# Optimization experiments

Measured on AMD Instinct MI355X. Metric: run time of the kernel, lower is better.

Reference implementation:

```python
import jax, jax.numpy as jnp
import numpy as np

NUM_CLASSES = 80
SCORE_THRESH = 0.5
NMS_THRESH = 0.5
TOP_K = 200  # max candidates kept per (image, class) before greedy NMS


def setup_inputs() -> dict:
    key = jax.random.key(0)
    k1, k2, k3 = jax.random.split(key, 3)
    B, A, HW, C = 8, 3, 5776, NUM_CLASSES  # 608-input YOLOv4 P3 level: 76*76
    # well-formed boxes in [0,1]: x1y1 + positive wh
    xy = jax.random.uniform(k1, (B, A, HW, 2)) * 0.8
    wh = jax.random.uniform(k2, (B, A, HW, 2)) * 0.2 + 0.01
    boxes = jnp.concatenate([xy, xy + wh], axis=-1)
    scores = jax.random.uniform(k3, (B, A, HW, C))
    return {"boxes": boxes, "scores": scores}


def _pairwise_iou(b):
    # b: [K, 4] (x1, y1, x2, y2) -> IoU matrix [K, K] (union mode)
    x1, y1, x2, y2 = b[:, 0], b[:, 1], b[:, 2], b[:, 3]
    area = (x2 - x1) * (y2 - y1)
    xx1 = jnp.maximum(x1[:, None], x1[None, :])
    yy1 = jnp.maximum(y1[:, None], y1[None, :])
    xx2 = jnp.minimum(x2[:, None], x2[None, :])
    yy2 = jnp.minimum(y2[:, None], y2[None, :])
    inter = jnp.maximum(0.0, xx2 - xx1) * jnp.maximum(0.0, yy2 - yy1)
    return inter / (area[:, None] + area[None, :] - inter)


def _nms_one(boxes, scores):
    # boxes: [N, 4], scores: [N] -> top-K candidates with greedy-NMS keep mask
    s = jnp.where(scores > SCORE_THRESH, scores, -jnp.inf)  # score threshold filter
    top_s, idx = jax.lax.top_k(s, TOP_K)                    # descending, like argsort()[::-1]
    b = boxes[idx]                                          # [K, 4]
    valid = jnp.isfinite(top_s)
    iou = _pairwise_iou(b)                                  # [K, K]

    def body(keep, i):
        # if box i survives, suppress all lower-scored boxes with IoU > thresh
        sup = keep[i] & (iou[i] > NMS_THRESH) & (jnp.arange(TOP_K) > i)
        return keep & ~sup, None

    keep, _ = jax.lax.scan(body, valid, jnp.arange(TOP_K))
    return b, top_s, keep


def reference(boxes, scores):
    B, A, HW, _ = boxes.shape
    C = scores.shape[-1]
    b = boxes.reshape(B, A * HW, 4)
    s = scores.reshape(B, A * HW, C)
    per_img = jax.vmap(lambda bb, ss: jax.vmap(_nms_one, in_axes=(None, 1))(bb, ss))
    boxes_k, scores_k, keep = per_img(b, s)  # [B,C,K,4], [B,C,K], [B,C,K]
    cls = jnp.broadcast_to(jnp.arange(C, dtype=boxes.dtype)[None, :, None], keep.shape)
    out_box = jnp.where(keep[..., None], boxes_k, 0.0)
    out_score = jnp.where(keep, scores_k, 0.0)
    out_cls = jnp.where(keep, cls, 0.0)
    # padded detections [B, C, K, 6] = (x1, y1, x2, y2, score, class_id)
    return jnp.concatenate([out_box, out_score[..., None], out_cls[..., None]], axis=-1)
```

## Files before the change

### kernel.cpp

```cpp
#include <hip/hip_runtime.h>
#include <stdint.h>

#define B_IMG  8
#define NANCH  17328
#define NCLS   80
#define TOPK   200
#define NTHR   256
#define NTHRB  512
#define CHUNK  64
#define NCHK   ((NANCH + CHUNK - 1) / CHUNK)
#define NCHKP  272
#define SLOT   12
#define NPOS   (NCHK * SLOT)
#define NBC    (B_IMG * NCLS)
#define THRESH_HI 0.98f

__device__ __forceinline__ void hist_add(float s, unsigned int* hist) {
  if (s > 0.5f) {
    unsigned int bin = (__float_as_uint(s) - 0x3F000000u) >> 15;
    if (bin > 255u) bin = 255u;
    atomicAdd(&hist[bin], 1u);
  }
}

__global__ __launch_bounds__(NTHR) void scatter_k(
    const float* __restrict__ scores,
    unsigned char* __restrict__ cnt2,
    unsigned long long* __restrict__ cand) {
  const int nb = blockIdx.x;
  const int b  = blockIdx.y;
  const int tid = threadIdx.x;
  const int wv = tid >> 6, lane = tid & 63;
  const int n0 = nb * CHUNK;

  __shared__ float tile[CHUNK][81];

  const int nrow = (NANCH - n0 < CHUNK) ? (NANCH - n0) : CHUNK;
  const int nf4 = nrow * (NCLS / 4);
  const float4* src4 = (const float4*)(scores + (size_t)(b * NANCH + n0) * NCLS);
  for (int f = tid; f < nf4; f += NTHR) {
    float4 v = src4[f];
    int n = f / 20, c4 = (f - n * 20) * 4;
    tile[n][c4] = v.x; tile[n][c4 + 1] = v.y;
    tile[n][c4 + 2] = v.z; tile[n][c4 + 3] = v.w;
  }
  __syncthreads();

  const bool rv = (lane < nrow);
  const unsigned long long lt = (1ull << lane) - 1ull;
  const int cbase = wv * 20;
#pragma unroll 4
  for (int cc = 0; cc < 20; ++cc) {
    const int c = cbase + cc;
    const int bc = b * NCLS + c;
    float s = rv ? tile[lane][c] : 0.f;
    const bool cd = (s > THRESH_HI);
    unsigned long long bal = __ballot(cd);
    if (cd) {
      unsigned int r = (unsigned int)__popcll(bal & lt);
      if (r < SLOT)
        cand[((size_t)bc * NCHK + nb) * SLOT + r] =
            ((unsigned long long)__float_as_uint(s) << 32) |
            (unsigned long long)(0xFFFFFFFFu - (unsigned int)(n0 + lane));
    }
    if (lane == 0)
      cnt2[(size_t)bc * NCHKP + nb] = (unsigned char)__popcll(bal);
  }
}

__global__ __launch_bounds__(NTHR) void select_k(
    const float* __restrict__ scores, const float* __restrict__ boxes,
    const unsigned char* __restrict__ cnt2, const unsigned long long* __restrict__ cand,
    float4* __restrict__ stagedBox, unsigned long long* __restrict__ stagedKey) {
  const int bc = blockIdx.x;
  const int b = bc / NCLS;
  const int c = bc - b * NCLS;
  const int tid = threadIdx.x;
  const int lane = tid & 63;
  const unsigned long long lt = (1ull << lane) - 1ull;

  __shared__ unsigned long long selk[512];
  __shared__ unsigned int hist[256];
  __shared__ unsigned int sh_cutbits;
  __shared__ int sh_sel, sh_bad;

  if (tid == 0) { sh_sel = 0; sh_bad = 0; }
  __syncthreads();

  const unsigned long long* cb0 = cand + (size_t)bc * NCHK * SLOT;
  const unsigned char* ct0 = cnt2 + (size_t)bc * NCHKP;
  for (int p = tid; p < NPOS; p += NTHR) {
    const int ch = p / SLOT;
    const int sl = p - ch * SLOT;
    unsigned int ci = (unsigned int)ct0[ch];
    if (sl == 0 && ci > SLOT) sh_bad = 1;
    unsigned long long k = 0ull;
    bool pred = (sl < (int)ci);
    if (pred) k = cb0[p];
    unsigned long long bal = __ballot(pred);
    if (bal) {
      int base0 = 0;
      if (lane == 0) base0 = atomicAdd(&sh_sel, (int)__popcll(bal));
      base0 = __shfl(base0, 0, 64);
      if (pred) {
        int pos = base0 + (int)__popcll(bal & lt);
        if (pos < 512) selk[pos] = k;
      }
    }
  }
  __syncthreads();

  int Msel = sh_sel;
  const bool fb = (sh_bad != 0) || (Msel < TOPK) || (Msel > 512);

  if (fb) {
    if (tid < 256) hist[tid] = 0u;
    if (tid == 0) sh_sel = 0;
    __syncthreads();
    const float* src = scores + (size_t)b * NANCH * NCLS + c;
    for (int i = tid; i < NANCH; i += NTHR) hist_add(src[(size_t)i * NCLS], hist);
    __syncthreads();
    if (tid == 0) {
      unsigned int acc = 0;
      int cut = 0;
      for (int bin = 255; bin >= 0; --bin) {
        acc += hist[bin];
        if (acc >= TOPK) { cut = bin; break; }
      }
      sh_cutbits = 0x3F000000u + ((unsigned int)cut << 15);
    }
    __syncthreads();
    const unsigned int cutbits = sh_cutbits;
    for (int i = tid; i < NANCH; i += NTHR) {
      float s = src[(size_t)i * NCLS];
      if (s > 0.5f && __float_as_uint(s) >= cutbits) {
        int slot = atomicAdd(&sh_sel, 1);
        if (slot < 512)
          selk[slot] = ((unsigned long long)__float_as_uint(s) << 32) |
                       (unsigned long long)(0xFFFFFFFFu - (unsigned int)i);
      }
    }
    __syncthreads();
    Msel = sh_sel; if (Msel > 512) Msel = 512;
  }

  const int S = (Msel <= 256) ? 256 : 512;
  for (int j = Msel + tid; j < S; j += NTHR) selk[j] = 0ull;

  for (int size = 2; size <= S; size <<= 1) {
    for (int st = size >> 1; st > 0; st >>= 1) {
      __syncthreads();
      for (int t = tid; t < (S >> 1); t += NTHR) {
        int lo = 2 * t - (t & (st - 1));
        int hi = lo + st;
        bool desc = ((lo & size) == 0);
        unsigned long long a = selk[lo], bb = selk[hi];
        if ((a < bb) == desc) { selk[lo] = bb; selk[hi] = a; }
      }
    }
  }
  __syncthreads();

  {
    unsigned long long key = selk[tid];
    int valid = (tid < TOPK) && (key != 0ull);
    unsigned int idx = 0xFFFFFFFFu - (unsigned int)(key & 0xFFFFFFFFull);
    float4 bx = make_float4(0.f, 0.f, 0.f, 0.f);
    if (valid) bx = ((const float4*)boxes)[(size_t)b * NANCH + idx];
    stagedBox[(size_t)bc * 256 + tid] = bx;
    stagedKey[(size_t)bc * 256 + tid] = valid ? key : 0ull;
  }
}

__global__ __launch_bounds__(NTHRB) void nms_k(
    const float4* __restrict__ stagedBox, const unsigned long long* __restrict__ stagedKey,
    float* __restrict__ out) {
  const int bc = blockIdx.x;
  const int c = bc - (bc / NCLS) * NCLS;
  const int tid = threadIdx.x;
  const int wv = tid >> 6, lane = tid & 63;

  __shared__ float sx1[256], sy1[256], sx2[256], sy2[256], sar[256], ssc[256];
  __shared__ int skeep[256];
  __shared__ __align__(16) unsigned long long sup[TOPK][4];
  __shared__ __align__(16) float eout[TOPK * 6];

  if (tid < 256) {
    unsigned long long key = stagedKey[(size_t)bc * 256 + tid];
    float4 bx = stagedBox[(size_t)bc * 256 + tid];
    int valid = (tid < TOPK) && (key != 0ull);
    sx1[tid] = bx.x; sy1[tid] = bx.y; sx2[tid] = bx.z; sy2[tid] = bx.w;
    sar[tid] = __fmul_rn(bx.z - bx.x, bx.w - bx.y);
    ssc[tid] = valid ? __uint_as_float((unsigned int)(key >> 32)) : 0.f;
    skeep[tid] = valid;
  }
  __syncthreads();

  {
    float jx1[4], jy1[4], jx2[4], jy2[4], ja[4];
#pragma unroll
    for (int r = 0; r < 4; ++r) {
      int j = (r << 6) | lane;
      jx1[r] = sx1[j]; jy1[r] = sy1[j]; jx2[r] = sx2[j]; jy2[r] = sy2[j];
      ja[r] = sar[j];
    }
    float nx1 = sx1[wv], ny1 = sy1[wv], nx2 = sx2[wv], ny2 = sy2[wv], na = sar[wv];
    for (int k = 0; k < 25; ++k) {
      const int i = (k << 3) + wv;
      const float xi1 = nx1, yi1 = ny1, xi2 = nx2, yi2 = ny2, ai = na;
      const int inx = i + 8;
      if (inx < TOPK) {
        nx1 = sx1[inx]; ny1 = sy1[inx]; nx2 = sx2[inx]; ny2 = sy2[inx];
        na = sar[inx];
      }
      const int d = i >> 6;
      const int il = i & 63;
      unsigned long long dmask = (il == 63) ? 0ull : ((~0ull) << (il + 1));
      if (d == 3) dmask &= 0xFFull;
      unsigned long long w[4];
#pragma unroll
      for (int r = 0; r < 4; ++r) {
        unsigned long long word = 0ull;
        if ((r << 6) + 63 > i) {
          const unsigned long long wmask =
              (r > d) ? ((r == 3) ? 0xFFull : ~0ull) : dmask;
          float xx1 = fmaxf(xi1, jx1[r]);
          float yy1 = fmaxf(yi1, jy1[r]);
          float xx2 = fminf(xi2, jx2[r]);
          float yy2 = fminf(yi2, jy2[r]);
          float iw = fmaxf(0.f, __fsub_rn(xx2, xx1));
          float ih = fmaxf(0.f, __fsub_rn(yy2, yy1));
          float inter = __fmul_rn(iw, ih);
          float denom = __fsub_rn(__fadd_rn(ai, ja[r]), inter);
          float i2 = __fadd_rn(inter, inter);
          word = __ballot(i2 > denom);
          unsigned long long gb =
              __ballot((i2 > denom) &&
                       (i2 <= __fmul_rn(denom, 1.0000005f))) & wmask;
          if (gb)
            word = __ballot(__fdiv_rn(inter, denom) > 0.5f);
          word &= wmask;
        }
        w[r] = word;
      }
      if (lane == 0) {
        ulonglong2* dst = (ulonglong2*)&sup[i][0];
        ulonglong2 t0; t0.x = w[0]; t0.y = w[1];
        ulonglong2 t1; t1.x = w[2]; t1.y = w[3];
        dst[0] = t0; dst[1] = t1;
      }
    }
  }
  __syncthreads();

  if (tid < 64) {
    unsigned long long k0 = __ballot(skeep[tid] != 0);
    unsigned long long k1 = __ballot(skeep[64 + tid] != 0);
    unsigned long long k2 = __ballot(skeep[128 + tid] != 0);
    unsigned long long k3 = __ballot(skeep[192 + tid] != 0);
#define NMS_SCAN_WORD(KW, BASE, CNT)                                     \
    _Pragma("unroll 8")                                                  \
    for (int li = 0; li < (CNT); ++li) {                                 \
      const ulonglong2* s2p =                                            \
          reinterpret_cast<const ulonglong2*>(&sup[(BASE) + li][0]);     \
      ulonglong2 sa = s2p[0];                                            \
      ulonglong2 sb = s2p[1];                                            \
      unsigned long long m = 0ull - ((KW >> li) & 1ull);                 \
      k0 &= ~(sa.x & m); k1 &= ~(sa.y & m);                              \
      k2 &= ~(sb.x & m); k3 &= ~(sb.y & m);                              \
    }
    NMS_SCAN_WORD(k0, 0, 64)
    NMS_SCAN_WORD(k1, 64, 64)
    NMS_SCAN_WORD(k2, 128, 64)
    NMS_SCAN_WORD(k3, 192, 8)
#undef NMS_SCAN_WORD
    skeep[tid]        = (int)((k0 >> tid) & 1ull);
    skeep[64 + tid]   = (int)((k1 >> tid) & 1ull);
    skeep[128 + tid]  = (int)((k2 >> tid) & 1ull);
    skeep[192 + tid]  = (int)((k3 >> tid) & 1ull);
  }
  __syncthreads();

  if (tid < TOPK) {
    int kp = skeep[tid];
    eout[tid * 6 + 0] = kp ? sx1[tid] : 0.f;
    eout[tid * 6 + 1] = kp ? sy1[tid] : 0.f;
    eout[tid * 6 + 2] = kp ? sx2[tid] : 0.f;
    eout[tid * 6 + 3] = kp ? sy2[tid] : 0.f;
    eout[tid * 6 + 4] = kp ? ssc[tid] : 0.f;
    eout[tid * 6 + 5] = kp ? (float)c : 0.f;
  }
  __syncthreads();

  float4* out4 = (float4*)(out + (size_t)bc * (TOPK * 6));
  const float4* e4 = (const float4*)eout;
  for (int f = tid; f < (TOPK * 6) / 4; f += NTHRB) out4[f] = e4[f];
}

__global__ __launch_bounds__(NTHR) void select_nms_k(
    const float* __restrict__ boxes, const float* __restrict__ scores,
    float* __restrict__ out) {
  const int blk = blockIdx.x;
  const int b = blk / NCLS;
  const int c = blk - b * NCLS;
  const int tid = threadIdx.x;

  __shared__ unsigned int hist[256];
  __shared__ unsigned long long keys[1024];
  __shared__ float sx1[TOPK], sy1[TOPK], sx2[TOPK], sy2[TOPK], sar[TOPK], ssc[TOPK];
  __shared__ int skeep[TOPK];
  __shared__ unsigned int sh_cutbits;
  __shared__ int sh_m;

  const float* src = scores + (size_t)b * NANCH * NCLS + c;

  for (int j = tid; j < 256; j += NTHR) hist[j] = 0;
  if (tid == 0) sh_m = 0;
  __syncthreads();

  for (int i = tid; i < NANCH; i += NTHR) hist_add(src[(size_t)i * NCLS], hist);
  __syncthreads();

  if (tid == 0) {
    unsigned int acc = 0;
    int cut = 0;
    for (int bin = 255; bin >= 0; --bin) {
      acc += hist[bin];
      if (acc >= TOPK) { cut = bin; break; }
    }
    sh_cutbits = 0x3F000000u + ((unsigned int)cut << 15);
  }
  __syncthreads();
  const unsigned int cutbits = sh_cutbits;

  for (int i = tid; i < NANCH; i += NTHR) {
    float s = src[(size_t)i * NCLS];
    if (s > 0.5f && __float_as_uint(s) >= cutbits) {
      int slot = atomicAdd(&sh_m, 1);
      if (slot < 1024)
        keys[slot] = ((unsigned long long)__float_as_uint(s) << 32) |
                     (unsigned long long)(0xFFFFFFFFu - (unsigned int)i);
    }
  }
  __syncthreads();
  int M = sh_m; if (M > 1024) M = 1024;
  for (int j = M + tid; j < 1024; j += NTHR) keys[j] = 0ull;

  for (int size = 2; size <= 1024; size <<= 1) {
    for (int st = size >> 1; st > 0; st >>= 1) {
      __syncthreads();
      for (int t = tid; t < 512; t += NTHR) {
        int lo = 2 * t - (t & (st - 1));
        int hi = lo + st;
        bool desc = ((lo & size) == 0);
        unsigned long long a = keys[lo], bb = keys[hi];
        if ((a < bb) == desc) { keys[lo] = bb; keys[hi] = a; }
      }
    }
  }
  __syncthreads();

  if (tid < TOPK) {
    unsigned long long key = keys[tid];
    int valid = (key != 0ull);
    float sc = __uint_as_float((unsigned int)(key >> 32));
    unsigned int idx = 0xFFFFFFFFu - (unsigned int)(key & 0xFFFFFFFFull);
    float4 bx = make_float4(0.f, 0.f, 0.f, 0.f);
    if (valid) bx = ((const float4*)boxes)[(size_t)b * NANCH + idx];
    sx1[tid] = bx.x; sy1[tid] = bx.y; sx2[tid] = bx.z; sy2[tid] = bx.w;
    sar[tid] = __fmul_rn(bx.z - bx.x, bx.w - bx.y);
    ssc[tid] = valid ? sc : 0.f;
    skeep[tid] = valid;
  }
  __syncthreads();

  if (tid < 64) {
    const int lane = tid;
    float x1v[4], y1v[4], x2v[4], y2v[4], av[4];
    int km = 0;
#pragma unroll
    for (int r = 0; r < 4; ++r) {
      int j = lane + (r << 6);
      if (j < TOPK) {
        x1v[r] = sx1[j]; y1v[r] = sy1[j]; x2v[r] = sx2[j]; y2v[r] = sy2[j];
        av[r] = sar[j];
        if (skeep[j]) km |= (1 << r);
      } else {
        x1v[r] = 0.f; y1v[r] = 0.f; x2v[r] = 0.f; y2v[r] = 0.f; av[r] = 0.f;
      }
    }
#pragma unroll
    for (int ri = 0; ri < 4; ++ri) {
      const int imax = (ri == 3) ? (TOPK - 192) : 64;
      for (int li = 0; li < imax; ++li) {
        const int i = (ri << 6) + li;
        int kmi = __shfl(km, li, 64);
        if (!((kmi >> ri) & 1)) continue;
        float xi1 = __shfl(x1v[ri], li, 64);
        float yi1 = __shfl(y1v[ri], li, 64);
        float xi2 = __shfl(x2v[ri], li, 64);
        float yi2 = __shfl(y2v[ri], li, 64);
        float ai  = __shfl(av[ri],  li, 64);
#pragma unroll
        for (int r = 0; r < 4; ++r) {
          int j = lane + (r << 6);
          if (j > i && j < TOPK && ((km >> r) & 1)) {
            float xx1 = fmaxf(xi1, x1v[r]);
            float yy1 = fmaxf(yi1, y1v[r]);
            float xx2 = fminf(xi2, x2v[r]);
            float yy2 = fminf(yi2, y2v[r]);
            float iw = fmaxf(0.f, __fsub_rn(xx2, xx1));
            float ih = fmaxf(0.f, __fsub_rn(yy2, yy1));
            float inter = __fmul_rn(iw, ih);
            float denom = __fsub_rn(__fadd_rn(ai, av[r]), inter);
            float iou = __fdiv_rn(inter, denom);
            if (iou > 0.5f) km &= ~(1 << r);
          }
        }
      }
    }
#pragma unroll
    for (int r = 0; r < 4; ++r) {
      int j = lane + (r << 6);
      if (j < TOPK) skeep[j] = (km >> r) & 1;
    }
  }
  __syncthreads();

  const size_t base = ((size_t)b * NCLS + c) * (TOPK * 6);
  for (int f = tid; f < TOPK * 6; f += NTHR) {
    int k = f / 6, comp = f - k * 6;
    float v = 0.f;
    if (skeep[k]) {
      switch (comp) {
        case 0: v = sx1[k]; break;
        case 1: v = sy1[k]; break;
        case 2: v = sx2[k]; break;
        case 3: v = sy2[k]; break;
        case 4: v = ssc[k]; break;
        default: v = (float)c; break;
      }
    }
    out[base + f] = v;
  }
}

extern "C" void kernel_launch(void* const* d_in, const int* in_sizes, int n_in,
                              void* d_out, int out_size, void* d_ws, size_t ws_size,
                              hipStream_t stream) {
  (void)in_sizes; (void)n_in; (void)out_size;
  const float* boxes  = (const float*)d_in[0];
  const float* scores = (const float*)d_in[1];
  float* out = (float*)d_out;

  const size_t need_c2 = (size_t)NBC * NCHKP;
  const size_t need_cd = (size_t)NBC * NCHK * SLOT * sizeof(uint64_t);
  const size_t need_sb = (size_t)NBC * 256 * sizeof(float4);
  const size_t need_sk = (size_t)NBC * 256 * sizeof(uint64_t);
  const size_t need = need_c2 + need_cd + need_sb + need_sk;

  if (ws_size >= need) {
    char* w = (char*)d_ws;
    unsigned char* cnt2           = (unsigned char*)w;       w += need_c2;
    unsigned long long* cand      = (unsigned long long*)w;  w += need_cd;
    float4* stagedBox             = (float4*)w;              w += need_sb;
    unsigned long long* stagedKey = (unsigned long long*)w;

    scatter_k<<<dim3(NCHK, B_IMG), NTHR, 0, stream>>>(scores, cnt2, cand);
    select_k<<<NBC, NTHR, 0, stream>>>(scores, boxes, cnt2, cand,
                                       stagedBox, stagedKey);
    nms_k<<<NBC, NTHRB, 0, stream>>>(stagedBox, stagedKey, out);
  } else {
    select_nms_k<<<NBC, NTHR, 0, stream>>>(boxes, scores, out);
  }
}
```

Before: 79.71 us.

## Split NMS into separate suppression-matrix build and scan/emit kernels

The fused NMS kernel, which used 640 blocks of 512 threads, is split in two. A new kernel builds the pairwise suppression bitmask rows in global memory using 4 blocks per (image, class), each handling an interleaved quarter of the rows. A second kernel loads the bitmask into shared memory, runs the greedy scan and writes the output. This raises parallelism for the IoU phase at the cost of an extra launch, a global round trip for the bitmask, and loading the boxes twice.

```diff
diff --git a/kernel.cpp b/kernel.cpp
--- a/kernel.cpp
+++ b/kernel.cpp
@@ -6,7 +6,6 @@
 #define NCLS   80
 #define TOPK   200
 #define NTHR   256
-#define NTHRB  512
 #define CHUNK  64
 #define NCHK   ((NANCH + CHUNK - 1) / CHUNK)
 #define NCHKP  272
@@ -172,84 +171,106 @@
   }
 }
 
-__global__ __launch_bounds__(NTHRB) void nms_k(
+__global__ __launch_bounds__(NTHR) void supbuild_k(
+    const float4* __restrict__ stagedBox,
+    unsigned long long* __restrict__ supg) {
+  const int blk = blockIdx.x;
+  const int h = blk & 3;
+  const int bc = blk >> 2;
+  const int tid = threadIdx.x;
+  const int wv = tid >> 6, lane = tid & 63;
+
+  __shared__ float sx1[256], sy1[256], sx2[256], sy2[256], sar[256];
+
+  if (tid < 256) {
+    float4 bx = stagedBox[(size_t)bc * 256 + tid];
+    sx1[tid] = bx.x; sy1[tid] = bx.y; sx2[tid] = bx.z; sy2[tid] = bx.w;
+    sar[tid] = __fmul_rn(bx.z - bx.x, bx.w - bx.y);
+  }
+  __syncthreads();
+
+  float jx1[4], jy1[4], jx2[4], jy2[4], ja[4];
+#pragma unroll
+  for (int r = 0; r < 4; ++r) {
+    int j = (r << 6) | lane;
+    jx1[r] = sx1[j]; jy1[r] = sy1[j]; jx2[r] = sx2[j]; jy2[r] = sy2[j];
+    ja[r] = sar[j];
+  }
+
+  const int i0 = 4 * wv + h;
+  float nx1 = sx1[i0], ny1 = sy1[i0], nx2 = sx2[i0], ny2 = sy2[i0], na = sar[i0];
+  for (int k = 0; k < 13; ++k) {
+    const int i = 16 * k + i0;
+    if (i >= TOPK) break;
+    const float xi1 = nx1, yi1 = ny1, xi2 = nx2, yi2 = ny2, ai = na;
+    const int inx = i + 16;
+    if (inx < TOPK) {
+      nx1 = sx1[inx]; ny1 = sy1[inx]; nx2 = sx2[inx]; ny2 = sy2[inx];
+      na = sar[inx];
+    }
+    const int d = i >> 6;
+    const int il = i & 63;
+    unsigned long long dmask = (il == 63) ? 0ull : ((~0ull) << (il + 1));
+    if (d == 3) dmask &= 0xFFull;
+    unsigned long long w[4];
+#pragma unroll
+    for (int r = 0; r < 4; ++r) {
+      unsigned long long word = 0ull;
+      if ((r << 6) + 63 > i) {
+        const unsigned long long wmask =
+            (r > d) ? ((r == 3) ? 0xFFull : ~0ull) : dmask;
+        float xx1 = fmaxf(xi1, jx1[r]);
+        float yy1 = fmaxf(yi1, jy1[r]);
+        float xx2 = fminf(xi2, jx2[r]);
+        float yy2 = fminf(yi2, jy2[r]);
+        float iw = fmaxf(0.f, __fsub_rn(xx2, xx1));
+        float ih = fmaxf(0.f, __fsub_rn(yy2, yy1));
+        float inter = __fmul_rn(iw, ih);
+        float denom = __fsub_rn(__fadd_rn(ai, ja[r]), inter);
+        float i2 = __fadd_rn(inter, inter);
+        word = __ballot(i2 > denom);
+        unsigned long long gb =
+            __ballot((i2 > denom) &&
+                     (i2 <= __fmul_rn(denom, 1.0000005f))) & wmask;
+        if (gb)
+          word = __ballot(__fdiv_rn(inter, denom) > 0.5f);
+        word &= wmask;
+      }
+      w[r] = word;
+    }
+    if (lane == 0) {
+      ulonglong2* dst = (ulonglong2*)(supg + ((size_t)bc * TOPK + i) * 4);
+      ulonglong2 t0; t0.x = w[0]; t0.y = w[1];
+      ulonglong2 t1; t1.x = w[2]; t1.y = w[3];
+      dst[0] = t0; dst[1] = t1;
+    }
+  }
+}
+
+__global__ __launch_bounds__(NTHR) void scanemit_k(
     const float4* __restrict__ stagedBox, const unsigned long long* __restrict__ stagedKey,
-    float* __restrict__ out) {
+    const unsigned long long* __restrict__ supg, float* __restrict__ out) {
   const int bc = blockIdx.x;
   const int c = bc - (bc / NCLS) * NCLS;
   const int tid = threadIdx.x;
-  const int wv = tid >> 6, lane = tid & 63;
-
-  __shared__ float sx1[256], sy1[256], sx2[256], sy2[256], sar[256], ssc[256];
+
+  __shared__ float sx1[256], sy1[256], sx2[256], sy2[256], ssc[256];
   __shared__ int skeep[256];
   __shared__ __align__(16) unsigned long long sup[TOPK][4];
   __shared__ __align__(16) float eout[TOPK * 6];
 
-  if (tid < 256) {
+  {
     unsigned long long key = stagedKey[(size_t)bc * 256 + tid];
     float4 bx = stagedBox[(size_t)bc * 256 + tid];
     int valid = (tid < TOPK) && (key != 0ull);
     sx1[tid] = bx.x; sy1[tid] = bx.y; sx2[tid] = bx.z; sy2[tid] = bx.w;
-    sar[tid] = __fmul_rn(bx.z - bx.x, bx.w - bx.y);
     ssc[tid] = valid ? __uint_as_float((unsigned int)(key >> 32)) : 0.f;
     skeep[tid] = valid;
   }
-  __syncthreads();
-
   {
-    float jx1[4], jy1[4], jx2[4], jy2[4], ja[4];
-#pragma unroll
-    for (int r = 0; r < 4; ++r) {
-      int j = (r << 6) | lane;
-      jx1[r] = sx1[j]; jy1[r] = sy1[j]; jx2[r] = sx2[j]; jy2[r] = sy2[j];
-      ja[r] = sar[j];
-    }
-    float nx1 = sx1[wv], ny1 = sy1[wv], nx2 = sx2[wv], ny2 = sy2[wv], na = sar[wv];
-    for (int k = 0; k < 25; ++k) {
-      const int i = (k << 3) + wv;
-      const float xi1 = nx1, yi1 = ny1, xi2 = nx2, yi2 = ny2, ai = na;
-      const int inx = i + 8;
-      if (inx < TOPK) {
-        nx1 = sx1[inx]; ny1 = sy1[inx]; nx2 = sx2[inx]; ny2 = sy2[inx];
-        na = sar[inx];
-      }
-      const int d = i >> 6;
-      const int il = i & 63;
-      unsigned long long dmask = (il == 63) ? 0ull : ((~0ull) << (il + 1));
-      if (d == 3) dmask &= 0xFFull;
-      unsigned long long w[4];
-#pragma unroll
-      for (int r = 0; r < 4; ++r) {
-        unsigned long long word = 0ull;
-        if ((r << 6) + 63 > i) {
-          const unsigned long long wmask =
-              (r > d) ? ((r == 3) ? 0xFFull : ~0ull) : dmask;
-          float xx1 = fmaxf(xi1, jx1[r]);
-          float yy1 = fmaxf(yi1, jy1[r]);
-          float xx2 = fminf(xi2, jx2[r]);
-          float yy2 = fminf(yi2, jy2[r]);
-          float iw = fmaxf(0.f, __fsub_rn(xx2, xx1));
-          float ih = fmaxf(0.f, __fsub_rn(yy2, yy1));
-          float inter = __fmul_rn(iw, ih);
-          float denom = __fsub_rn(__fadd_rn(ai, ja[r]), inter);
-          float i2 = __fadd_rn(inter, inter);
-          word = __ballot(i2 > denom);
-          unsigned long long gb =
-              __ballot((i2 > denom) &&
-                       (i2 <= __fmul_rn(denom, 1.0000005f))) & wmask;
-          if (gb)
-            word = __ballot(__fdiv_rn(inter, denom) > 0.5f);
-          word &= wmask;
-        }
-        w[r] = word;
-      }
-      if (lane == 0) {
-        ulonglong2* dst = (ulonglong2*)&sup[i][0];
-        ulonglong2 t0; t0.x = w[0]; t0.y = w[1];
-        ulonglong2 t1; t1.x = w[2]; t1.y = w[3];
-        dst[0] = t0; dst[1] = t1;
-      }
-    }
+    const ulonglong2* src = (const ulonglong2*)(supg + (size_t)bc * TOPK * 4);
+    ulonglong2* dst = (ulonglong2*)&sup[0][0];
+    for (int f = tid; f < TOPK * 2; f += NTHR) dst[f] = src[f];
   }
   __syncthreads();
 
@@ -294,7 +315,7 @@
 
   float4* out4 = (float4*)(out + (size_t)bc * (TOPK * 6));
   const float4* e4 = (const float4*)eout;
-  for (int f = tid; f < (TOPK * 6) / 4; f += NTHRB) out4[f] = e4[f];
+  for (int f = tid; f < (TOPK * 6) / 4; f += NTHR) out4[f] = e4[f];
 }
 
 __global__ __launch_bounds__(NTHR) void select_nms_k(
@@ -457,19 +478,22 @@
   const size_t need_cd = (size_t)NBC * NCHK * SLOT * sizeof(uint64_t);
   const size_t need_sb = (size_t)NBC * 256 * sizeof(float4);
   const size_t need_sk = (size_t)NBC * 256 * sizeof(uint64_t);
-  const size_t need = need_c2 + need_cd + need_sb + need_sk;
+  const size_t need_sp = (size_t)NBC * TOPK * 4 * sizeof(uint64_t);
+  const size_t need = need_c2 + need_cd + need_sb + need_sk + need_sp;
 
   if (ws_size >= need) {
     char* w = (char*)d_ws;
     unsigned char* cnt2           = (unsigned char*)w;       w += need_c2;
     unsigned long long* cand      = (unsigned long long*)w;  w += need_cd;
     float4* stagedBox             = (float4*)w;              w += need_sb;
-    unsigned long long* stagedKey = (unsigned long long*)w;
+    unsigned long long* stagedKey = (unsigned long long*)w;  w += need_sk;
+    unsigned long long* supg      = (unsigned long long*)w;
 
     scatter_k<<<dim3(NCHK, B_IMG), NTHR, 0, stream>>>(scores, cnt2, cand);
     select_k<<<NBC, NTHR, 0, stream>>>(scores, boxes, cnt2, cand,
                                        stagedBox, stagedKey);
-    nms_k<<<NBC, NTHRB, 0, stream>>>(stagedBox, stagedKey, out);
+    supbuild_k<<<NBC * 4, NTHR, 0, stream>>>(stagedBox, supg);
+    scanemit_k<<<NBC, NTHR, 0, stream>>>(stagedBox, stagedKey, supg, out);
   } else {
     select_nms_k<<<NBC, NTHR, 0, stream>>>(boxes, scores, out);
   }
```

Result: no change. 78.69 us (-1.3%).
